# Performance work log

Hardware: AMD Instinct MI355X
Metric: run time of the kernel (lower is better)

The kernel has to match this reference:

```python
import jax, jax.numpy as jnp
import numpy as np
import math

B, S, D, H, DFF = 2, 2048, 1024, 16, 4096
DK = D // H
EPS = 1e-6


def setup_inputs() -> dict:
    key = jax.random.key(0)
    ks = jax.random.split(key, 12)
    s = 0.02
    return {
        "x": jax.random.normal(ks[0], (B, S, D), jnp.float32),
        "mask": jnp.ones((B, S), jnp.int32),
        "wq": jax.random.normal(ks[1], (D, D), jnp.float32) * s,
        "bq": jnp.zeros((D,), jnp.float32),
        "wk": jax.random.normal(ks[2], (D, D), jnp.float32) * s,
        "bk": jnp.zeros((D,), jnp.float32),
        "wv": jax.random.normal(ks[3], (D, D), jnp.float32) * s,
        "bv": jnp.zeros((D,), jnp.float32),
        "wo": jax.random.normal(ks[4], (D, D), jnp.float32) * s,
        "bo": jnp.zeros((D,), jnp.float32),
        "g1": jnp.ones((D,), jnp.float32),
        "b1": jnp.zeros((D,), jnp.float32),
        "g2": jnp.ones((D,), jnp.float32),
        "b2": jnp.zeros((D,), jnp.float32),
        "w1": jax.random.normal(ks[5], (DFF, D), jnp.float32) * s,
        "bf1": jnp.zeros((DFF,), jnp.float32),
        "w2": jax.random.normal(ks[6], (D, DFF), jnp.float32) * s,
        "bf2": jnp.zeros((D,), jnp.float32),
    }


def _gelu(x):
    # x * 0.5 * (1 + erf(x / sqrt(2))) -- exact erf-based GELU as in source
    return x * 0.5 * (1.0 + jax.lax.erf(x * (1.0 / math.sqrt(2.0))))


def _layernorm(x, gamma, beta):
    # torch.std uses unbiased (ddof=1); eps is OUTSIDE the sqrt in the source
    mean = jnp.mean(x, axis=-1, keepdims=True)
    std = jnp.std(x, axis=-1, keepdims=True, ddof=1)
    return gamma * (x - mean) / (std + EPS) + beta


def _block(x, mask, wq, bq, wk, bk, wv, bv, wo, bo, g1, b1, g2, b2, w1, bf1, w2, bf2):
    # multi-head attention (dropout is identity in eval mode)
    q = (x @ wq.T + bq).reshape(B, S, H, DK).transpose(0, 2, 1, 3)  # bhsd
    k = (x @ wk.T + bk).reshape(B, S, H, DK).transpose(0, 2, 1, 3)
    v = (x @ wv.T + bv).reshape(B, S, H, DK).transpose(0, 2, 1, 3)
    scores = jnp.einsum("bhsd,bhtd->bhst", q, k) / math.sqrt(DK)
    scores = jnp.where(mask[:, None, None, :] == 0, -1e9, scores)
    attn = jax.nn.softmax(scores, axis=-1)
    cv = jnp.einsum("bhst,bhtd->bhsd", attn, v)
    cv = cv.transpose(0, 2, 1, 3).reshape(B, S, D)
    hd = cv @ wo.T + bo
    # residual + norm1
    hd = _layernorm(x + hd, g1, b1)
    # position-wise FFN with erf GELU
    ff = _gelu(hd @ w1.T + bf1) @ w2.T + bf2
    return _layernorm(hd + ff, g2, b2)


def reference(x, mask, wq, bq, wk, bk, wv, bv, wo, bo, g1, b1, g2, b2, w1, bf1, w2, bf2):
    return _block(x, mask, wq, bq, wk, bk, wv, bv, wo, bo, g1, b1, g2, b2, w1, bf1, w2, bf2)
```

## Files before the change

### kernel.cpp

```cpp
#include <hip/hip_runtime.h>
#include <hip/hip_bf16.h>

#define B_   2
#define S_   2048
#define D_   1024
#define H_   16
#define DK_  64
#define DFF_ 4096
#define M_   (B_*S_)

typedef unsigned short u16;
typedef __attribute__((ext_vector_type(8))) short short8;
typedef __attribute__((ext_vector_type(4))) short bf16x4;
typedef __attribute__((ext_vector_type(4))) float floatx4;

__device__ __forceinline__ u16 f2bf(float f) {
    union { float f; unsigned u; } v; v.f = f;
    unsigned r = v.u + 0x7fffu + ((v.u >> 16) & 1u);
    return (u16)(r >> 16);
}
__device__ __forceinline__ u16 f2bf_fast(float f) {
    __hip_bfloat16 h = __float2bfloat16(f);
    return *reinterpret_cast<u16*>(&h);
}
__device__ __forceinline__ float b2f(u16 u) {
    union { unsigned u; float f; } v; v.u = ((unsigned)u) << 16; return v.f;
}
__device__ __forceinline__ float exp2_fast(float f) {
    return __builtin_amdgcn_exp2f(f);
}
__device__ __forceinline__ void g2l16(const u16* g, u16* l) {
    __builtin_amdgcn_global_load_lds((const __attribute__((address_space(1))) void*)g,
                                     (__attribute__((address_space(3))) void*)l,
                                     16, 0, 0);
}
__device__ __forceinline__ unsigned lds_off(const void* p) {
    return (unsigned)(unsigned long long)p;
}

#define TRB16(dst, va, IMM)                                                    \
    asm volatile("ds_read_b64_tr_b16 %0, %1 offset:" #IMM                      \
                 : "=v"(dst) : "v"(va))

__global__ __launch_bounds__(256) void cvt_all(
    const float* __restrict__ x,  const float* __restrict__ wq,
    const float* __restrict__ wk, const float* __restrict__ wv,
    const float* __restrict__ wo, const float* __restrict__ w1,
    const float* __restrict__ w2,
    const float* __restrict__ bq, const float* __restrict__ bk,
    const float* __restrict__ bv, const int* __restrict__ mask,
    u16* __restrict__ xb, u16* __restrict__ wqkvb, u16* __restrict__ wob,
    u16* __restrict__ w1b, u16* __restrict__ w2b,
    float* __restrict__ bqkv, float* __restrict__ mbias) {
    for (int i = blockIdx.x * 256 + threadIdx.x; i < 4201472;
         i += gridDim.x * 256) {
        if (i < 4194304) {
            const float* s; u16* d; int off;
            if (i < 1048576)      { s = x;  d = xb;    off = i; }
            else if (i < 1310720) { s = wq; d = wqkvb; off = i - 1048576; }
            else if (i < 1572864) { s = wk; d = wqkvb + 1048576; off = i - 1310720; }
            else if (i < 1835008) { s = wv; d = wqkvb + 2097152; off = i - 1572864; }
            else if (i < 2097152) { s = wo; d = wob;   off = i - 1835008; }
            else if (i < 3145728) { s = w1; d = w1b;   off = i - 2097152; }
            else                  { s = w2; d = w2b;   off = i - 3145728; }
            float4 v = reinterpret_cast<const float4*>(s)[off];
            ushort4 o;
            o.x = f2bf(v.x); o.y = f2bf(v.y); o.z = f2bf(v.z); o.w = f2bf(v.w);
            reinterpret_cast<ushort4*>(d)[off] = o;
        } else {
            int j = i - 4194304;
            if (j < 3 * D_) {
                float v = (j < D_) ? bq[j] : (j < 2 * D_) ? bk[j - D_] : bv[j - 2 * D_];
                bqkv[j] = v;
            } else {
                int k = j - 3 * D_;
                mbias[k] = (mask[k] == 0) ? -1.44269504e9f : 0.0f;
            }
        }
    }
}

template <int EPI>
__global__ __launch_bounds__(512, 2) void gemm256_bt(const u16* __restrict__ A,
                                                     const u16* __restrict__ Bw,
                                                     const float* __restrict__ bias,
                                                     u16* __restrict__ Cb,
                                                     int N, int K) {
    __shared__ alignas(16) u16 sA[2][2][8192];
    __shared__ alignas(16) u16 sB[2][2][8192];
    const int tid = threadIdx.x;
    const int wid = tid >> 6, lane = tid & 63;
    const int lrow = lane & 15, lgrp = lane >> 4;
    const int wm = wid >> 2, wn = wid & 3;
    const int z = blockIdx.z;
    const int Kc = K / gridDim.z;
    const int zbase = z * Kc;

    const int nbx = gridDim.x, nby = gridDim.y;
    const int nwg = nbx * nby;
    const int orig = blockIdx.y * nbx + blockIdx.x;
    const int qd = nwg >> 3, rr = nwg & 7, xc = orig & 7, oi = orig >> 3;
    const int swz = (xc < rr ? xc * (qd + 1) : rr * (qd + 1) + (xc - rr) * qd) + oi;
    const int m0 = (swz / nby) * 256, n0 = (swz % nby) * 256;

    const u16* Ab = A + (size_t)m0 * K + zbase;
    const u16* Bb = Bw + (size_t)n0 * K + zbase;
    const int T = Kc >> 6;

    const int c0 = (wid * 2 + 0) * 64 + lane;
    const int c1 = (wid * 2 + 1) * 64 + lane;
    const int r0 = c0 >> 3, g0 = c0 & 7;
    const int r1 = c1 >> 3, g1 = c1 & 7;
    const size_t so0 = (size_t)r0 * K + (size_t)((g0 ^ (r0 & 7)) * 8);
    const size_t so1 = (size_t)r1 * K + (size_t)((g1 ^ (r1 & 7)) * 8);
    const int d0 = (wid * 2 + 0) * 512;
    const int d1 = (wid * 2 + 1) * 512;

    auto stageA = [&](int par, int half, int kt) {
        const u16* src = Ab + (size_t)(half * 128) * K + kt * 64;
        g2l16(src + so0, &sA[par][half][d0]);
        g2l16(src + so1, &sA[par][half][d1]);
    };
    auto stageB = [&](int par, int half, int kt) {
        const u16* src = Bb + (size_t)(half * 128) * K + kt * 64;
        g2l16(src + so0, &sB[par][half][d0]);
        g2l16(src + so1, &sB[par][half][d1]);
    };

    stageA(0, 0, 0); stageA(0, 1, 0);
    stageB(0, 0, 0); stageB(0, 1, 0);
    if (T > 1) { stageB(1, 0, 1); stageB(1, 1, 1); }
    asm volatile("s_waitcnt vmcnt(4)" ::: "memory");
    asm volatile("s_barrier" ::: "memory");

    floatx4 acc[8][4] = {};
    const int rbase = (wn & 1) * 64;
    const int bhalf = wn >> 1;

    for (int t = 0; t < T; t++) {
        const int par = t & 1;
        const char* baseA = (const char*)&sA[par][wm][0];
        const char* baseB = (const char*)&sB[par][bhalf][0];
        short8 bfr[4][2];
#pragma unroll
        for (int ph = 0; ph < 4; ph++) {
            if (ph == 0) {
#pragma unroll
                for (int nj = 0; nj < 4; nj++) {
                    int rb = rbase + nj * 16 + lrow;
#pragma unroll
                    for (int kk = 0; kk < 2; kk++) {
                        int off = rb * 128 + (((kk * 4 + lgrp) ^ (lrow & 7)) * 16);
                        bfr[nj][kk] = *reinterpret_cast<const short8*>(baseB + off);
                    }
                }
            }
            short8 af[2][2];
#pragma unroll
            for (int a = 0; a < 2; a++) {
                int ra = (2 * ph + a) * 16 + lrow;
#pragma unroll
                for (int kk = 0; kk < 2; kk++) {
                    int off = ra * 128 + (((kk * 4 + lgrp) ^ (lrow & 7)) * 16);
                    af[a][kk] = *reinterpret_cast<const short8*>(baseA + off);
                }
            }
            if (ph == 0) { if (t + 1 < T) stageA(par ^ 1, 0, t + 1); }
            if (ph == 1) { if (t + 1 < T) stageA(par ^ 1, 1, t + 1); }
            if (ph == 2) { if (t + 2 < T) stageB(par, 0, t + 2); }
            if (ph == 3) { if (t + 2 < T) stageB(par, 1, t + 2); }

            asm volatile("s_barrier" ::: "memory");
            asm volatile("s_waitcnt lgkmcnt(0)" ::: "memory");
            __builtin_amdgcn_sched_barrier(0);

            __builtin_amdgcn_s_setprio(1);
#pragma unroll
            for (int a = 0; a < 2; a++)
#pragma unroll
                for (int nj = 0; nj < 4; nj++) {
                    acc[2 * ph + a][nj] = __builtin_amdgcn_mfma_f32_16x16x32_bf16(
                        af[a][0], bfr[nj][0], acc[2 * ph + a][nj], 0, 0, 0);
                    acc[2 * ph + a][nj] = __builtin_amdgcn_mfma_f32_16x16x32_bf16(
                        af[a][1], bfr[nj][1], acc[2 * ph + a][nj], 0, 0, 0);
                }
            __builtin_amdgcn_s_setprio(0);

            if (ph == 3) {
                if (t >= T - 3) asm volatile("s_waitcnt vmcnt(0)" ::: "memory");
                else            asm volatile("s_waitcnt vmcnt(4)" ::: "memory");
            }
            asm volatile("s_barrier" ::: "memory");
        }
    }

    u16* Co = (EPI == 1) ? Cb + (size_t)z * M_ * N : Cb;
#pragma unroll
    for (int mi = 0; mi < 8; mi++) {
        int row = m0 + wm * 128 + mi * 16 + lgrp * 4;
#pragma unroll
        for (int nj = 0; nj < 4; nj++) {
            int col = n0 + wn * 64 + nj * 16 + lrow;
            float bc = (EPI != 1 || z == 0) ? bias[col] : 0.0f;
#pragma unroll
            for (int j = 0; j < 4; j++) {
                float v = acc[mi][nj][j] + bc;
                if (EPI == 2) v = 0.5f * v * (1.0f + erff(v * 0.70710678118654752f));
                Co[(size_t)(row + j) * N + col] = f2bf(v);
            }
        }
    }
}

__global__ __launch_bounds__(256) void attn_kernel(const u16* __restrict__ QKV,
                                                   const float* __restrict__ mbias,
                                                   u16* __restrict__ O) {
    const int SD = 3 * D_;
    __shared__ alignas(16) u16 ktL[2][4096];
    __shared__ alignas(16) u16 vtL[2][4096];
    __shared__ alignas(16) u16 pL[4][1024];

    const int orig = blockIdx.y * gridDim.x + blockIdx.x;
    const int swz = (orig & 7) * 128 + (orig >> 3);
    const int qt = swz & 31, bh = swz >> 5;
    const int b = bh >> 4, h = bh & 15;

    const int tid = threadIdx.x, wid = tid >> 6, lane = tid & 63;
    const int lrow = lane & 15, lgrp = lane >> 4;

    const u16* Qp = QKV + h * DK_;
    const u16* Kp = QKV + D_ + h * DK_;
    const u16* Vp = QKV + 2 * D_ + h * DK_;
    const float* mbrow = mbias + b * S_;

    const int qr = qt * 64 + wid * 16 + lrow;
    const u16* qrow = Qp + (size_t)(b * S_ + qr) * SD;
    short8 aq0 = *reinterpret_cast<const short8*>(qrow + lgrp * 8);
    short8 aq1 = *reinterpret_cast<const short8*>(qrow + 32 + lgrp * 8);

    const u16* kq[2];
    const u16* vq[2];
#pragma unroll
    for (int i = 0; i < 2; i++) {
        int s = wid * 2 + i;
        int q8 = s * 64 + lane;
        int krow = q8 >> 3, kcb = q8 & 7;
        kq[i] = Kp + (size_t)(b * S_ + krow) * SD + ((kcb ^ (krow & 7)) * 8);
        int o = s * 512 + lane * 8;
        int vk = ((o >> 6) & 7) * 8 + ((o >> 9) & 1) * 4 + ((o >> 4) & 3);
        int vd = (o >> 10) * 16 + (o & 8);
        vq[i] = Vp + (size_t)(b * S_ + vk) * SD + vd;
    }

    auto issue = [&](int bufIdx) {
        u16* kb_ = ktL[bufIdx];
        u16* vb_ = vtL[bufIdx];
#pragma unroll
        for (int i = 0; i < 2; i++) {
            int s = wid * 2 + i;
            g2l16(kq[i], kb_ + s * 512);
            g2l16(vq[i], vb_ + s * 512);
            kq[i] += 64 * SD;
            vq[i] += 64 * SD;
        }
    };

    floatx4 accO[4] = {};
    float mrun = -1e30f, lrun = 0.f;
    const float SC2 = 0.18033688011112042f;

    issue(0);
    int cur = 0;
    for (int t = 0; t < S_ / 64; t++) {
        const int kv0 = t * 64;
        if (t < S_ / 64 - 1) {
            issue(cur ^ 1);
            asm volatile("s_waitcnt vmcnt(4)" ::: "memory");
        } else {
            asm volatile("s_waitcnt vmcnt(0)" ::: "memory");
        }
        __builtin_amdgcn_s_barrier();
        asm volatile("" ::: "memory");

        const u16* ktc = ktL[cur];
        const unsigned vva = lds_off(vtL[cur]) + lane * 8;

        float4 mb[4];
#pragma unroll
        for (int ni = 0; ni < 4; ni++)
            mb[ni] = *reinterpret_cast<const float4*>(mbrow + kv0 + ni * 16 + lgrp * 4);

        floatx4 st[4];
        __builtin_amdgcn_s_setprio(1);
#pragma unroll
        for (int ni = 0; ni < 4; ni++) {
            int row = ni * 16 + lrow;
            int off0 = (row * 128 + lgrp * 16) ^ ((lrow & 7) << 4);
            int off1 = (row * 128 + 64 + lgrp * 16) ^ ((lrow & 7) << 4);
            short8 bk0 = *reinterpret_cast<const short8*>((const char*)ktc + off0);
            short8 bk1 = *reinterpret_cast<const short8*>((const char*)ktc + off1);
            floatx4 z = {0.f, 0.f, 0.f, 0.f};
            z = __builtin_amdgcn_mfma_f32_16x16x32_bf16(bk0, aq0, z, 0, 0, 0);
            z = __builtin_amdgcn_mfma_f32_16x16x32_bf16(bk1, aq1, z, 0, 0, 0);
            st[ni] = z;
        }
        __builtin_amdgcn_s_setprio(0);

        bf16x4 vt0[4], vt1[4], vt2[4], vt3[4];
#pragma unroll
        for (int nd = 0; nd < 4; nd++) {
            unsigned a = vva + nd * 2048;
            TRB16(vt0[nd], a, 0);
            TRB16(vt1[nd], a, 1024);
            TRB16(vt2[nd], a, 512);
            TRB16(vt3[nd], a, 1536);
        }

        float pm[4][4];
#pragma unroll
        for (int ni = 0; ni < 4; ni++) {
            const float* mbp = reinterpret_cast<const float*>(&mb[ni]);
#pragma unroll
            for (int j = 0; j < 4; j++)
                pm[ni][j] = fmaf(st[ni][j], SC2, mbp[j]);
        }
        float pmax = pm[0][0];
#pragma unroll
        for (int ni = 0; ni < 4; ni++)
#pragma unroll
            for (int j = 0; j < 4; j++) pmax = fmaxf(pmax, pm[ni][j]);
        pmax = fmaxf(pmax, __shfl_xor(pmax, 16, 64));
        pmax = fmaxf(pmax, __shfl_xor(pmax, 32, 64));

        bool upd = !__all(pmax - mrun <= 11.5f);
        float fac = 1.0f;
        if (upd) {
            float mn = fmaxf(mrun, pmax);
            fac = exp2_fast(mrun - mn);
            mrun = mn;
        }

        float p[4][4];
        float s = 0.f;
#pragma unroll
        for (int ni = 0; ni < 4; ni++)
#pragma unroll
            for (int j = 0; j < 4; j++) {
                float e = exp2_fast(pm[ni][j] - mrun);
                p[ni][j] = e;
                s += e;
            }
        s += __shfl_xor(s, 16, 64);
        s += __shfl_xor(s, 32, 64);
        lrun = lrun * fac + s;

#pragma unroll
        for (int ni = 0; ni < 4; ni++) {
            bf16x4 pw;
#pragma unroll
            for (int j = 0; j < 4; j++) pw[j] = (short)f2bf_fast(p[ni][j]);
            unsigned woff = (unsigned)((lrow * 128 + ni * 32 + lgrp * 8) ^ ((lrow & 7) << 4));
            *reinterpret_cast<bf16x4*>((char*)pL[wid] + woff) = pw;
        }

        if (upd) {
            float f0 = __shfl(fac, lgrp * 4 + 0, 64);
            float f1 = __shfl(fac, lgrp * 4 + 1, 64);
            float f2 = __shfl(fac, lgrp * 4 + 2, 64);
            float f3 = __shfl(fac, lgrp * 4 + 3, 64);
#pragma unroll
            for (int nd = 0; nd < 4; nd++) {
                floatx4 tt = accO[nd];
                tt[0] *= f0; tt[1] *= f1; tt[2] *= f2; tt[3] *= f3;
                accO[nd] = tt;
            }
        }

        asm volatile("s_waitcnt lgkmcnt(0)" ::: "memory");
        __builtin_amdgcn_sched_barrier(0);

        unsigned ra0 = (unsigned)((lrow * 128 + lgrp * 16) ^ ((lrow & 7) << 4));
        unsigned ra1 = (unsigned)((lrow * 128 + 64 + lgrp * 16) ^ ((lrow & 7) << 4));
        short8 ap0 = *reinterpret_cast<const short8*>((const char*)pL[wid] + ra0);
        short8 ap1 = *reinterpret_cast<const short8*>((const char*)pL[wid] + ra1);

        __builtin_amdgcn_s_setprio(1);
#pragma unroll
        for (int nd = 0; nd < 4; nd++) {
            short8 bv0 = __builtin_shufflevector(vt0[nd], vt1[nd], 0, 1, 2, 3, 4, 5, 6, 7);
            short8 bv1 = __builtin_shufflevector(vt2[nd], vt3[nd], 0, 1, 2, 3, 4, 5, 6, 7);
            accO[nd] = __builtin_amdgcn_mfma_f32_16x16x32_bf16(ap0, bv0, accO[nd], 0, 0, 0);
            accO[nd] = __builtin_amdgcn_mfma_f32_16x16x32_bf16(ap1, bv1, accO[nd], 0, 0, 0);
        }
        __builtin_amdgcn_s_setprio(0);

        asm volatile("" ::: "memory");
        __builtin_amdgcn_s_barrier();
        cur ^= 1;
    }

    float linv = 1.0f / lrun;
    float li[4];
#pragma unroll
    for (int j = 0; j < 4; j++) li[j] = __shfl(linv, lgrp * 4 + j, 64);
#pragma unroll
    for (int nd = 0; nd < 4; nd++)
#pragma unroll
        for (int j = 0; j < 4; j++) {
            int r = lgrp * 4 + j;
            float v = accO[nd][j] * li[j];
            O[(size_t)(b * S_ + qt * 64 + wid * 16 + r) * D_ + h * DK_ + nd * 16 + lrow] =
                f2bf_fast(v);
        }
}

__global__ __launch_bounds__(256) void ln_bf(const float* __restrict__ X,
                                             const u16* __restrict__ R0,
                                             const u16* __restrict__ R1,
                                             const u16* __restrict__ R2,
                                             const u16* __restrict__ R3,
                                             const float* __restrict__ gam,
                                             const float* __restrict__ bet,
                                             float* __restrict__ outf,
                                             u16* __restrict__ outb) {
    __shared__ float ws1[4], ws2[4];
    const int row = blockIdx.x, tid = threadIdx.x;
    const size_t ro = (size_t)row * D_;
    float4 v = reinterpret_cast<const float4*>(X + ro)[tid];
    {
        ushort4 r = reinterpret_cast<const ushort4*>(R0 + ro)[tid];
        v.x += b2f(r.x); v.y += b2f(r.y); v.z += b2f(r.z); v.w += b2f(r.w);
    }
    {
        ushort4 r = reinterpret_cast<const ushort4*>(R1 + ro)[tid];
        v.x += b2f(r.x); v.y += b2f(r.y); v.z += b2f(r.z); v.w += b2f(r.w);
    }
    {
        ushort4 r = reinterpret_cast<const ushort4*>(R2 + ro)[tid];
        v.x += b2f(r.x); v.y += b2f(r.y); v.z += b2f(r.z); v.w += b2f(r.w);
    }
    {
        ushort4 r = reinterpret_cast<const ushort4*>(R3 + ro)[tid];
        v.x += b2f(r.x); v.y += b2f(r.y); v.z += b2f(r.z); v.w += b2f(r.w);
    }

    float s = v.x + v.y + v.z + v.w;
#pragma unroll
    for (int m = 32; m >= 1; m >>= 1) s += __shfl_xor(s, m, 64);
    if ((tid & 63) == 0) ws1[tid >> 6] = s;
    __syncthreads();
    float mean = (ws1[0] + ws1[1] + ws1[2] + ws1[3]) * (1.f / D_);

    float4 d; d.x = v.x - mean; d.y = v.y - mean; d.z = v.z - mean; d.w = v.w - mean;
    float q = d.x * d.x + d.y * d.y + d.z * d.z + d.w * d.w;
#pragma unroll
    for (int m = 32; m >= 1; m >>= 1) q += __shfl_xor(q, m, 64);
    if ((tid & 63) == 0) ws2[tid >> 6] = q;
    __syncthreads();
    float var = (ws2[0] + ws2[1] + ws2[2] + ws2[3]) * (1.f / (D_ - 1));
    float inv = 1.f / (sqrtf(var) + 1e-6f);

    const float4 g = reinterpret_cast<const float4*>(gam)[tid];
    const float4 bb = reinterpret_cast<const float4*>(bet)[tid];
    float4 o;
    o.x = g.x * d.x * inv + bb.x;
    o.y = g.y * d.y * inv + bb.y;
    o.z = g.z * d.z * inv + bb.z;
    o.w = g.w * d.w * inv + bb.w;
    if (outf) reinterpret_cast<float4*>(outf + ro)[tid] = o;
    if (outb) {
        ushort4 ob;
        ob.x = f2bf(o.x); ob.y = f2bf(o.y); ob.z = f2bf(o.z); ob.w = f2bf(o.w);
        reinterpret_cast<ushort4*>(outb + ro)[tid] = ob;
    }
}

extern "C" void kernel_launch(void* const* d_in, const int* in_sizes, int n_in,
                              void* d_out, int out_size, void* d_ws, size_t ws_size,
                              hipStream_t stream) {
    const float* x    = (const float*)d_in[0];
    const int*   mask = (const int*)d_in[1];
    const float* wq   = (const float*)d_in[2];
    const float* bq   = (const float*)d_in[3];
    const float* wk   = (const float*)d_in[4];
    const float* bk   = (const float*)d_in[5];
    const float* wv   = (const float*)d_in[6];
    const float* bv   = (const float*)d_in[7];
    const float* wo   = (const float*)d_in[8];
    const float* bo   = (const float*)d_in[9];
    const float* g1   = (const float*)d_in[10];
    const float* b1   = (const float*)d_in[11];
    const float* g2   = (const float*)d_in[12];
    const float* b2   = (const float*)d_in[13];
    const float* w1   = (const float*)d_in[14];
    const float* bf1  = (const float*)d_in[15];
    const float* w2   = (const float*)d_in[16];
    const float* bf2  = (const float*)d_in[17];
    float* out = (float*)d_out;

    char* ws = (char*)d_ws;
    const size_t MB = 1u << 20;
    u16*   xb    = (u16*)  (ws + 0 * MB);
    u16*   wqkvb = (u16*)  (ws + 8 * MB);
    u16*   qkvb  = (u16*)  (ws + 14 * MB);
    u16*   cvb   = (u16*)  (ws + 64 * MB);
    u16*   pp    = (u16*)  (ws + 0 * MB);
    u16*   qpart = (u16*)  (ws + 0 * MB);
    u16*   wob   = (u16*)  (ws + 72 * MB);
    u16*   w1b   = (u16*)  (ws + 74 * MB);
    u16*   w2b   = (u16*)  (ws + 82 * MB);
    float* bqkv  = (float*)(ws + 90 * MB);
    float* mbias = (float*)(ws + 90 * MB + 65536);
    float* hdf   = (float*)(ws + 91 * MB);
    u16*   hdb   = (u16*)  (ws + 107 * MB);
    u16*   ff1b  = (u16*)  (ws + 115 * MB);

    cvt_all<<<2048, 256, 0, stream>>>(x, wq, wk, wv, wo, w1, w2,
                                      bq, bk, bv, mask,
                                      xb, wqkvb, wob, w1b, w2b, bqkv, mbias);

    gemm256_bt<0><<<dim3(M_ / 256, 3 * D_ / 256, 1), 512, 0, stream>>>(
        xb, wqkvb, bqkv, qkvb, 3 * D_, D_);

    attn_kernel<<<dim3(S_ / 64, B_ * H_), 256, 0, stream>>>(qkvb, mbias, cvb);

    gemm256_bt<1><<<dim3(M_ / 256, D_ / 256, 4), 512, 0, stream>>>(
        cvb, wob, bo, pp, D_, D_);

    ln_bf<<<M_, 256, 0, stream>>>(x, pp, pp + (size_t)M_ * D_,
                                  pp + 2 * (size_t)M_ * D_,
                                  pp + 3 * (size_t)M_ * D_,
                                  g1, b1, hdf, hdb);

    gemm256_bt<2><<<dim3(M_ / 256, DFF_ / 256, 1), 512, 0, stream>>>(
        hdb, w1b, bf1, ff1b, DFF_, D_);

    gemm256_bt<1><<<dim3(M_ / 256, D_ / 256, 4), 512, 0, stream>>>(
        ff1b, w2b, bf2, qpart, D_, DFF_);

    ln_bf<<<M_, 256, 0, stream>>>(hdf, qpart, qpart + (size_t)M_ * D_,
                                  qpart + 2 * (size_t)M_ * D_,
                                  qpart + 3 * (size_t)M_ * D_,
                                  g2, b2, out, nullptr);
}
```

Measured before the change: 408.1 us.

## Double attention query tile to 128 rows with 8 waves sharing K/V tiles

The attention kernel now runs 512 threads per block, with 8 waves each owning 16 query rows, so a block covers 128 queries instead of 64. Each K/V tile staged in LDS is reused by twice as many query rows, which halves global K/V traffic and the number of staging loads per wave. In exchange the grid has half as many blocks (512) and occupancy per CU may drop, since more LDS and threads are needed per block.

New measurement: 374.2 us. 1.09x faster.

```diff
diff --git a/kernel.cpp b/kernel.cpp
--- a/kernel.cpp
+++ b/kernel.cpp
@@ -212,17 +212,17 @@
     }
 }
 
-__global__ __launch_bounds__(256) void attn_kernel(const u16* __restrict__ QKV,
+__global__ __launch_bounds__(512) void attn_kernel(const u16* __restrict__ QKV,
                                                    const float* __restrict__ mbias,
                                                    u16* __restrict__ O) {
     const int SD = 3 * D_;
     __shared__ alignas(16) u16 ktL[2][4096];
     __shared__ alignas(16) u16 vtL[2][4096];
-    __shared__ alignas(16) u16 pL[4][1024];
+    __shared__ alignas(16) u16 pL[8][1024];
 
     const int orig = blockIdx.y * gridDim.x + blockIdx.x;
-    const int swz = (orig & 7) * 128 + (orig >> 3);
-    const int qt = swz & 31, bh = swz >> 5;
+    const int swz = (orig & 7) * 64 + (orig >> 3);
+    const int qt = swz & 15, bh = swz >> 4;
     const int b = bh >> 4, h = bh & 15;
 
     const int tid = threadIdx.x, wid = tid >> 6, lane = tid & 63;
@@ -233,36 +233,24 @@
     const u16* Vp = QKV + 2 * D_ + h * DK_;
     const float* mbrow = mbias + b * S_;
 
-    const int qr = qt * 64 + wid * 16 + lrow;
+    const int qr = qt * 128 + wid * 16 + lrow;
     const u16* qrow = Qp + (size_t)(b * S_ + qr) * SD;
     short8 aq0 = *reinterpret_cast<const short8*>(qrow + lgrp * 8);
     short8 aq1 = *reinterpret_cast<const short8*>(qrow + 32 + lgrp * 8);
 
-    const u16* kq[2];
-    const u16* vq[2];
-#pragma unroll
-    for (int i = 0; i < 2; i++) {
-        int s = wid * 2 + i;
-        int q8 = s * 64 + lane;
-        int krow = q8 >> 3, kcb = q8 & 7;
-        kq[i] = Kp + (size_t)(b * S_ + krow) * SD + ((kcb ^ (krow & 7)) * 8);
-        int o = s * 512 + lane * 8;
-        int vk = ((o >> 6) & 7) * 8 + ((o >> 9) & 1) * 4 + ((o >> 4) & 3);
-        int vd = (o >> 10) * 16 + (o & 8);
-        vq[i] = Vp + (size_t)(b * S_ + vk) * SD + vd;
-    }
+    const int q8 = wid * 64 + lane;
+    const int krow = q8 >> 3, kcb = q8 & 7;
+    const u16* kq = Kp + (size_t)(b * S_ + krow) * SD + ((kcb ^ (krow & 7)) * 8);
+    const int ov = wid * 512 + lane * 8;
+    const int vk = ((ov >> 6) & 7) * 8 + ((ov >> 9) & 1) * 4 + ((ov >> 4) & 3);
+    const int vd = (ov >> 10) * 16 + (ov & 8);
+    const u16* vq = Vp + (size_t)(b * S_ + vk) * SD + vd;
 
     auto issue = [&](int bufIdx) {
-        u16* kb_ = ktL[bufIdx];
-        u16* vb_ = vtL[bufIdx];
-#pragma unroll
-        for (int i = 0; i < 2; i++) {
-            int s = wid * 2 + i;
-            g2l16(kq[i], kb_ + s * 512);
-            g2l16(vq[i], vb_ + s * 512);
-            kq[i] += 64 * SD;
-            vq[i] += 64 * SD;
-        }
+        g2l16(kq, &ktL[bufIdx][wid * 512]);
+        g2l16(vq, &vtL[bufIdx][wid * 512]);
+        kq += 64 * SD;
+        vq += 64 * SD;
     };
 
     floatx4 accO[4] = {};
@@ -275,7 +263,7 @@
         const int kv0 = t * 64;
         if (t < S_ / 64 - 1) {
             issue(cur ^ 1);
-            asm volatile("s_waitcnt vmcnt(4)" ::: "memory");
+            asm volatile("s_waitcnt vmcnt(2)" ::: "memory");
         } else {
             asm volatile("s_waitcnt vmcnt(0)" ::: "memory");
         }
@@ -409,7 +397,7 @@
         for (int j = 0; j < 4; j++) {
             int r = lgrp * 4 + j;
             float v = accO[nd][j] * li[j];
-            O[(size_t)(b * S_ + qt * 64 + wid * 16 + r) * D_ + h * DK_ + nd * 16 + lrow] =
+            O[(size_t)(b * S_ + qt * 128 + wid * 16 + r) * D_ + h * DK_ + nd * 16 + lrow] =
                 f2bf_fast(v);
         }
 }
@@ -522,7 +510,7 @@
     gemm256_bt<0><<<dim3(M_ / 256, 3 * D_ / 256, 1), 512, 0, stream>>>(
         xb, wqkvb, bqkv, qkvb, 3 * D_, D_);
 
-    attn_kernel<<<dim3(S_ / 64, B_ * H_), 256, 0, stream>>>(qkvb, mbias, cvb);
+    attn_kernel<<<dim3(S_ / 128, B_ * H_), 512, 0, stream>>>(qkvb, mbias, cvb);
 
     gemm256_bt<1><<<dim3(M_ / 256, D_ / 256, 4), 512, 0, stream>>>(
         cvb, wob, bo, pp, D_, D_);
```
